# Performance work log

Measured on AMD Instinct MI355X. Metric: run time of the kernel, lower is better.

Reference implementation:

```python
import jax, jax.numpy as jnp
import numpy as np


def setup_inputs() -> dict:
    key = jax.random.key(0)
    ks = jax.random.split(key, 12)
    B, C, H, W = 8, 256, 64, 64
    inter = C // 8
    s = 0.05  # weight scale keeps q.k logits in a stable softmax range
    f32 = jnp.float32
    x = jax.random.normal(ks[0], (B, C, H, W), f32)
    Wq = jax.random.normal(ks[1], (inter, C), f32) * s
    bq = jnp.zeros((inter,), f32)
    Wk = jax.random.normal(ks[2], (inter, C), f32) * s
    bk = jnp.zeros((inter,), f32)
    Wv = jax.random.normal(ks[3], (C, C), f32) * s
    bv = jnp.zeros((C,), f32)
    gamma = jnp.full((1,), 0.5, f32)  # learnable residual scale (init 0 in torch; 0.5 exercises the path)
    Wg1 = jax.random.normal(ks[4], (inter, C), f32) * s
    bg1 = jnp.zeros((inter,), f32)
    Wg2 = jax.random.normal(ks[5], (C, inter), f32) * s
    bg2 = jnp.zeros((C,), f32)
    return {"x": x, "Wq": Wq, "bq": bq, "Wk": Wk, "bk": bk, "Wv": Wv, "bv": bv,
            "gamma": gamma, "Wg1": Wg1, "bg1": bg1, "Wg2": Wg2, "bg2": bg2}


def reference(x, Wq, bq, Wk, bk, Wv, bv, gamma, Wg1, bg1, Wg2, bg2):
    B, C, H, W = x.shape
    N = H * W
    xf = x.reshape(B, C, N)  # [B,C,N]
    # 1x1 convs == per-pixel linear projections
    q = jnp.einsum('oc,bcn->bon', Wq, xf) + bq[None, :, None]  # [B,inter,N]
    k = jnp.einsum('oc,bcn->bon', Wk, xf) + bk[None, :, None]  # [B,inter,N]
    v = jnp.einsum('oc,bcn->bon', Wv, xf) + bv[None, :, None]  # [B,C,N]
    # attention[b,n,m] = softmax_m( q[b,:,n] . k[b,:,m] )
    attn = jax.nn.softmax(jnp.einsum('bin,bim->bnm', q, k), axis=-1)  # [B,N,N]
    # out[b,c,n] = sum_m v[b,c,m] * attn[b,n,m]
    out = jnp.einsum('bcm,bnm->bcn', v, attn)  # [B,C,N]
    out = gamma[0] * out + xf
    # gated global pooling branch: GAP -> 1x1 conv -> ReLU -> 1x1 conv -> Sigmoid
    gp = xf.mean(axis=-1)  # [B,C]
    h = jax.nn.relu(jnp.einsum('oc,bc->bo', Wg1, gp) + bg1)  # [B,inter]
    ga = jax.nn.sigmoid(jnp.einsum('co,bo->bc', Wg2, h) + bg2)  # [B,C]
    out = out * ga[:, :, None] + out
    return out.reshape(B, C, H, W)
```

## Files before the change

kernel.cpp:

```cpp
#include <hip/hip_runtime.h>

typedef unsigned short u16;
typedef unsigned int   u32;
typedef short s16x4 __attribute__((ext_vector_type(4)));
typedef u16 u16x4 __attribute__((ext_vector_type(4)));
typedef u16 u16x8 __attribute__((ext_vector_type(8)));
typedef __bf16 bf16x8 __attribute__((ext_vector_type(8)));
typedef float f32x4 __attribute__((ext_vector_type(4)));
typedef float f32x2 __attribute__((ext_vector_type(2)));
typedef u32 u32x2v __attribute__((ext_vector_type(2)));
typedef u32 u32x4v __attribute__((ext_vector_type(4)));

#define NB 8
#define NC 256
#define NI 32
#define NN 4096
#define LOG2E 1.4426950408889634f
#define POFF 64.0f

#define OW_Q   0
#define OB_Q   8192
#define OW_K   8224
#define OB_K   16416
#define OW_V   16448
#define OB_V   81984
#define OGAM   82240
#define OW_G1  82248
#define OB_G1  90440
#define OW_G2  90472
#define OB_G2  98664
#define WTOT   98920

__device__ __forceinline__ float bf2f(u16 v) {
    u32 u = ((u32)v) << 16;
    return __builtin_bit_cast(float, u);
}
__device__ __forceinline__ u16 f2bf(float f) {
    u32 u = __builtin_bit_cast(u32, f);
    u32 lsb = (u >> 16) & 1u;
    u += 0x7fffu + lsb;
    return (u16)(u >> 16);
}
__device__ __forceinline__ u32 cvtpk_bf16(float lo, float hi) {
    u32 r;
    asm("v_cvt_pk_bf16_f32 %0, %1, %2" : "=v"(r) : "v"(lo), "v"(hi));
    return r;
}
__device__ __forceinline__ u16 f2bf_hw(float f) {
    u32 r;
    asm("v_cvt_pk_bf16_f32 %0, %1, %1" : "=v"(r) : "v"(f));
    return (u16)r;
}
__device__ __forceinline__ void permswap32(u32& a, u32& b) {
#if __has_builtin(__builtin_amdgcn_permlane32_swap)
    auto r = __builtin_amdgcn_permlane32_swap(a, b, false, false);
    a = (u32)r[0]; b = (u32)r[1];
#else
    int ln = (int)(threadIdx.x & 63);
    u32 a2 = (u32)__shfl_xor((int)a, 32, 64);
    u32 b2 = (u32)__shfl_xor((int)b, 32, 64);
    u32 na = (ln < 32) ? a : b2;
    u32 nb = (ln < 32) ? a2 : b;
    a = na; b = nb;
#endif
}
__device__ __forceinline__ void permswap16(u32& a, u32& b) {
#if __has_builtin(__builtin_amdgcn_permlane16_swap)
    auto r = __builtin_amdgcn_permlane16_swap(a, b, false, false);
    a = (u32)r[0]; b = (u32)r[1];
#else
    int q = (int)((threadIdx.x >> 4) & 1);
    u32 az = (u32)__shfl_xor((int)a, 16, 64);
    u32 bz = (u32)__shfl_xor((int)b, 16, 64);
    u32 na = q ? bz : a;
    u32 nb = q ? b  : az;
    a = na; b = nb;
#endif
}
__device__ __forceinline__ bool is_f32_mode(const void* graw) {
    return ((const u16*)graw)[0] == 0;
}

__global__ __launch_bounds__(256) void convert_kernel(
    const void* x,  const void* Wq, const void* bq, const void* Wk, const void* bk,
    const void* Wv, const void* bv, const void* gamma, const void* Wg1, const void* bg1,
    const void* Wg2, const void* bg2, float* __restrict__ xf, float* __restrict__ wbuf,
    u16* __restrict__ wbf, float* __restrict__ gp)
{
    bool f32m = is_f32_mode(gamma);
    int blk = blockIdx.x, t = threadIdx.x;
    if (blk < 2048) {
        int base = blk * 4096 + t * 16;
        float s = 0.f;
        if (f32m) {
            const float* xs = (const float*)x;
#pragma unroll
            for (int k = 0; k < 4; ++k) {
                f32x4 a = *(const f32x4*)(xs + base + k * 4);
                s += (a[0] + a[1]) + (a[2] + a[3]);
            }
        } else {
            const u16* xs = (const u16*)x;
#pragma unroll
            for (int k = 0; k < 2; ++k) {
                u16x8 a = *(const u16x8*)(xs + base + k * 8);
#pragma unroll
                for (int j = 0; j < 8; ++j) s += bf2f(a[j]);
            }
        }
#pragma unroll
        for (int off = 1; off <= 32; off <<= 1) s += __shfl_xor(s, off, 64);
        __shared__ float ws[4];
        if ((t & 63) == 0) ws[t >> 6] = s;
        __syncthreads();
        if (t == 0) gp[blk] = (ws[0] + ws[1] + ws[2] + ws[3]) * (1.0f / NN);
        return;
    }
    if (blk < 2080) {
        int tid = (blk - 2048) * 256 + t;
        const int off[12] = {OW_Q, OB_Q, OW_K, OB_K, OW_V, OB_V, OGAM, OW_G1, OB_G1, OW_G2, OB_G2, WTOT};
        const int len[11] = {8192, 32, 8192, 32, 65536, 256, 1, 8192, 32, 8192, 256};
        const void* srcs[11] = {Wq, bq, Wk, bk, Wv, bv, gamma, Wg1, bg1, Wg2, bg2};
        for (int w = tid; w < WTOT; w += 32 * 256) {
            int seg = 0;
#pragma unroll
            for (int i = 1; i < 11; ++i) if (w >= off[i]) seg = i;
            int idx = w - off[seg];
            float val = 0.f;
            if (idx < len[seg])
                val = f32m ? ((const float*)srcs[seg])[idx] : bf2f(((const u16*)srcs[seg])[idx]);
            wbuf[w] = val;
        }
        return;
    }
    int tid = (blk - 2080) * 256 + t;
    for (int w = tid; w < 320 * 256; w += 10 * 256) {
        int row = w >> 8, c = w & 255;
        const void* src; int idx; float scale = 1.f;
        if (row < 32)      { src = Wq; idx = row * 256 + c; scale = LOG2E; }
        else if (row < 64) { src = Wk; idx = (row - 32) * 256 + c; }
        else               { src = Wv; idx = (row - 64) * 256 + c; }
        float val = f32m ? ((const float*)src)[idx] : bf2f(((const u16*)src)[idx]);
        wbf[w] = f2bf(val * scale);
    }
}

__global__ __launch_bounds__(256) void proj_kernel(
    const void* xr, const float* __restrict__ xf, const void* graw,
    const float* __restrict__ wbuf, const u16* __restrict__ wbf,
    u16* __restrict__ qt, u16* __restrict__ kt, u16* __restrict__ v)
{
    __shared__ __attribute__((aligned(16))) u16 xs[64][264];

    bool f32m = is_f32_mode(graw);

    int t    = threadIdx.x;
    int lane = t & 63;
    int wave = t >> 6;
    int b    = blockIdx.x >> 6;
    int m0   = (blockIdx.x & 63) << 6;
    int l15  = lane & 15;
    int quad = lane >> 4;

    {
        int c0 = wave * 64;
        if (f32m) {
            const float* xb = (const float*)xr + (size_t)b * NC * NN + m0 + lane;
#pragma unroll
            for (int ci = 0; ci < 64; ci += 4) {
                int c = c0 + ci;
                float a0 = xb[(size_t)(c    ) * NN];
                float a1 = xb[(size_t)(c + 1) * NN];
                float a2 = xb[(size_t)(c + 2) * NN];
                float a3 = xb[(size_t)(c + 3) * NN];
                u32x2v p2;
                p2.x = cvtpk_bf16(a0, a1);
                p2.y = cvtpk_bf16(a2, a3);
                *(u32x2v*)&xs[lane][c] = p2;
            }
        } else {
            const u16* xb = (const u16*)xr + (size_t)b * NC * NN + m0 + lane;
#pragma unroll
            for (int ci = 0; ci < 64; ci += 4) {
                int c = c0 + ci;
                u16x4 p4;
                p4[0] = xb[(size_t)(c    ) * NN];
                p4[1] = xb[(size_t)(c + 1) * NN];
                p4[2] = xb[(size_t)(c + 2) * NN];
                p4[3] = xb[(size_t)(c + 3) * NN];
                *(u16x4*)&xs[lane][c] = p4;
            }
        }
    }
    __syncthreads();

    const f32x4 zero4 = {};
    f32x4 acc[5][4];
#pragma unroll
    for (int i = 0; i < 5; ++i)
#pragma unroll
        for (int mt = 0; mt < 4; ++mt) acc[i][mt] = zero4;

    int obase = wave * 80;
    const u16* wb = wbf + (size_t)(obase + l15) * 256 + quad * 8;

    bf16x8 af[5];
#pragma unroll
    for (int i = 0; i < 5; ++i)
        af[i] = *(const bf16x8*)(wb + (size_t)(i * 16) * 256);

#pragma unroll
    for (int kc = 0; kc < 8; ++kc) {
        bf16x8 afn[5], bfr[4];
        if (kc < 7) {
#pragma unroll
            for (int i = 0; i < 5; ++i)
                afn[i] = *(const bf16x8*)(wb + (size_t)(i * 16) * 256 + (kc + 1) * 32);
        }
#pragma unroll
        for (int mt = 0; mt < 4; ++mt)
            bfr[mt] = *(const bf16x8*)&xs[mt * 16 + l15][kc * 32 + quad * 8];
#pragma unroll
        for (int i = 0; i < 5; ++i)
#pragma unroll
            for (int mt = 0; mt < 4; ++mt)
                acc[i][mt] = __builtin_amdgcn_mfma_f32_16x16x32_bf16(af[i], bfr[mt], acc[i][mt], 0, 0, 0);
        if (kc < 7) {
#pragma unroll
            for (int i = 0; i < 5; ++i) af[i] = afn[i];
        }
    }

    __syncthreads();

    if (wave == 0) {
#pragma unroll
        for (int i = 0; i < 4; ++i) {
#pragma unroll
            for (int mt = 0; mt < 4; ++mt) {
                float tv[4];
#pragma unroll
                for (int r = 0; r < 4; ++r) {
                    int o = i * 16 + quad * 4 + r;
                    float bias = (o < 32) ? LOG2E * wbuf[OB_Q + o] : wbuf[OB_K + o - 32];
                    tv[r] = acc[i][mt][r] + bias;
                }
                u32x2v p2;
                p2.x = cvtpk_bf16(tv[0], tv[1]);
                p2.y = cvtpk_bf16(tv[2], tv[3]);
                *(u32x2v*)&xs[mt * 16 + l15][i * 16 + quad * 4] = p2;
            }
        }
        int m = m0 + lane;
        u16* qrow = qt + (size_t)(b * NN + m) * NI;
        u16* krow = kt + (size_t)(b * NN + m) * NI;
#pragma unroll
        for (int j = 0; j < 4; ++j) *(u16x8*)(qrow + j * 8) = *(const u16x8*)&xs[lane][j * 8];
#pragma unroll
        for (int j = 0; j < 4; ++j) *(u16x8*)(krow + j * 8) = *(const u16x8*)&xs[lane][32 + j * 8];
#pragma unroll
        for (int mt = 0; mt < 4; ++mt) {
#pragma unroll
            for (int r = 0; r < 4; ++r) {
                int c = quad * 4 + r;
                v[(size_t)(b * NC + c) * NN + m0 + mt * 16 + l15] = f2bf_hw(acc[4][mt][r] + wbuf[OB_V + c]);
            }
        }
    } else {
#pragma unroll
        for (int i = 0; i < 5; ++i) {
#pragma unroll
            for (int mt = 0; mt < 4; ++mt) {
#pragma unroll
                for (int r = 0; r < 4; ++r) {
                    int c = wave * 80 + i * 16 + quad * 4 + r - 64;
                    v[(size_t)(b * NC + c) * NN + m0 + mt * 16 + l15] = f2bf_hw(acc[i][mt][r] + wbuf[OB_V + c]);
                }
            }
        }
    }
}

__global__ __launch_bounds__(256) void gate_kernel(
    const float* __restrict__ gp, const float* __restrict__ wbuf, float* __restrict__ gmul)
{
    int b = blockIdx.x;
    int t = threadIdx.x;
    __shared__ float gps[NC];
    __shared__ float hs[NI];
    gps[t] = gp[b * NC + t];
    __syncthreads();
    if (t < NI) {
        float a = wbuf[OB_G1 + t];
        for (int c = 0; c < NC; ++c) a += wbuf[OW_G1 + t * NC + c] * gps[c];
        hs[t] = a > 0.f ? a : 0.f;
    }
    __syncthreads();
    float a = wbuf[OB_G2 + t];
#pragma unroll
    for (int i = 0; i < NI; ++i) a += wbuf[OW_G2 + t * NI + i] * hs[i];
    float sig = 1.f / (1.f + __expf(-a));
    gmul[b * NC + t] = 1.f + sig;
}

__global__ __launch_bounds__(512, 4) void flash_kernel(
    const u16* __restrict__ qt, const u16* __restrict__ kt, const u16* __restrict__ v,
    const void* xr, const float* __restrict__ xf, const void* graw,
    const float* __restrict__ wbuf, const float* __restrict__ gmul, void* outp)
{
    __shared__ __attribute__((aligned(16))) u16 vs[2][2][NC][40];

    bool f32m = is_f32_mode(graw);

    int t    = threadIdx.x;
    int lane = t & 63;
    int wave = t >> 6;
    int b    = blockIdx.x & 7;
    int nblk = (blockIdx.x >> 3) << 6;
    int n0   = nblk + (wave >> 1) * 16;
    int c0   = (wave & 1) * 128;
    int l15  = lane & 15;
    int quad = lane >> 4;

    const f32x4 mneg = {-POFF, -POFF, -POFF, -POFF};

    bf16x8 qf = *(const bf16x8*)(qt + (size_t)(b * NN + n0 + l15) * NI + quad * 8);

    f32x4 acc[8];
#pragma unroll
    for (int ct = 0; ct < 8; ++ct) acc[ct] = f32x4{};
    f32x2 psum2 = {};

    int sc = t >> 2;
    int sm = (t & 3) * 8;
    const u16* vb0 = v + (size_t)(b * NC + sc) * NN + sm;
    const u16* vb1 = v + (size_t)(b * NC + sc + 128) * NN + sm;
    const u16* ktb = kt + (size_t)(b * NN + l15) * NI + quad * 8;

    u16x8 sr0, sr1, sr2, sr3;
    sr0 = *(const u16x8*)(vb0);        sr1 = *(const u16x8*)(vb1);
    sr2 = *(const u16x8*)(vb0 + 32);   sr3 = *(const u16x8*)(vb1 + 32);
    *(u16x8*)&vs[0][0][sc][sm]       = sr0;
    *(u16x8*)&vs[0][0][sc + 128][sm] = sr1;
    *(u16x8*)&vs[0][1][sc][sm]       = sr2;
    *(u16x8*)&vs[0][1][sc + 128][sm] = sr3;
    sr0 = *(const u16x8*)(vb0 + 64);   sr1 = *(const u16x8*)(vb1 + 64);
    sr2 = *(const u16x8*)(vb0 + 96);   sr3 = *(const u16x8*)(vb1 + 96);
    bf16x8 ktA[2], ktB[2];
    ktA[0] = *(const bf16x8*)(ktb);
    ktA[1] = *(const bf16x8*)(ktb + (size_t)16 * NI);
    ktB[0] = *(const bf16x8*)(ktb + (size_t)32 * NI);
    ktB[1] = *(const bf16x8*)(ktb + (size_t)48 * NI);
    __syncthreads();

    for (int it = 0; it < 64; ++it) {
        int p = it & 1;
        bool wmore = (it < 63);
        bool lmore = (it < 62);

        if (wmore) {
            *(u16x8*)&vs[p ^ 1][0][sc][sm]       = sr0;
            *(u16x8*)&vs[p ^ 1][0][sc + 128][sm] = sr1;
            *(u16x8*)&vs[p ^ 1][1][sc][sm]       = sr2;
            *(u16x8*)&vs[p ^ 1][1][sc + 128][sm] = sr3;
        }
        if (lmore) {
            int cb = it * 64 + 128;
            sr0 = *(const u16x8*)(vb0 + cb);
            sr1 = *(const u16x8*)(vb1 + cb);
            sr2 = *(const u16x8*)(vb0 + cb + 32);
            sr3 = *(const u16x8*)(vb1 + cb + 32);
        }

#pragma unroll
        for (int h = 0; h < 2; ++h) {
            bf16x8* ktX = (h == 0) ? ktA : ktB;

            f32x4 sf[2];
#pragma unroll
            for (int mt = 0; mt < 2; ++mt)
                sf[mt] = __builtin_amdgcn_mfma_f32_16x16x32_bf16(ktX[mt], qf, mneg, 0, 0, 0);

            bf16x8 va8[8];
#pragma unroll
            for (int ct = 0; ct < 8; ++ct)
                va8[ct] = *(const bf16x8*)&vs[p][h][c0 + ct * 16 + l15][quad * 8];

            if (wmore) {
                int mg = it * 64 + 64 + h * 32;
                ktX[0] = *(const bf16x8*)(ktb + (size_t)mg * NI);
                ktX[1] = *(const bf16x8*)(ktb + (size_t)(mg + 16) * NI);
            }

            float pp[2][4];
#pragma unroll
            for (int mt = 0; mt < 2; ++mt)
#pragma unroll
                for (int r = 0; r < 4; ++r)
                    pp[mt][r] = __builtin_amdgcn_exp2f(sf[mt][r]);
            f32x2 t0; t0.x = pp[0][0]; t0.y = pp[0][1];
            f32x2 t1; t1.x = pp[0][2]; t1.y = pp[0][3];
            f32x2 t2; t2.x = pp[1][0]; t2.y = pp[1][1];
            f32x2 t3; t3.x = pp[1][2]; t3.y = pp[1][3];
            psum2 += (t0 + t1) + (t2 + t3);
            u32 A0 = cvtpk_bf16(pp[0][0], pp[0][1]);
            u32 A1 = cvtpk_bf16(pp[0][2], pp[0][3]);
            u32 B0 = cvtpk_bf16(pp[1][0], pp[1][1]);
            u32 B1 = cvtpk_bf16(pp[1][2], pp[1][3]);
            permswap32(A0, B0); permswap16(A0, B0);
            permswap32(A1, B1); permswap16(A1, B1);
            u32x4v f; f.x = A0; f.y = A1; f.z = B0; f.w = B1;
            bf16x8 pfr8 = __builtin_bit_cast(bf16x8, f);

#pragma unroll
            for (int ct = 0; ct < 8; ++ct)
                acc[ct] = __builtin_amdgcn_mfma_f32_16x16x32_bf16(va8[ct], pfr8, acc[ct], 0, 0, 0);
        }

        __syncthreads();
    }

    float s = psum2.x + psum2.y;
    s += __shfl_xor(s, 16, 64);
    s += __shfl_xor(s, 32, 64);
    float inv = 1.f / s;
    float gam = wbuf[OGAM];
    int n = n0 + l15;

#pragma unroll
    for (int ct = 0; ct < 8; ++ct) {
        int cb = c0 + ct * 16 + quad * 4;
        f32x4 gm4 = *(const f32x4*)&gmul[b * NC + cb];
#pragma unroll
        for (int r = 0; r < 4; ++r) {
            size_t off = (size_t)(b * NC + cb + r) * NN + n;
            float xv = f32m ? ((const float*)xr)[off] : bf2f(((const u16*)xr)[off]);
            float val = (gam * acc[ct][r] * inv + xv) * gm4[r];
            if (f32m) ((float*)outp)[off] = val;
            else      ((u16*)outp)[off]  = f2bf_hw(val);
        }
    }
}

extern "C" void kernel_launch(void* const* d_in, const int* in_sizes, int n_in,
                              void* d_out, int out_size, void* d_ws, size_t ws_size,
                              hipStream_t stream)
{
    const void* x     = d_in[0];
    const void* Wq    = d_in[1];
    const void* bq    = d_in[2];
    const void* Wk    = d_in[3];
    const void* bk    = d_in[4];
    const void* Wv    = d_in[5];
    const void* bvp   = d_in[6];
    const void* gamma = d_in[7];
    const void* Wg1   = d_in[8];
    const void* bg1   = d_in[9];
    const void* Wg2   = d_in[10];
    const void* bg2   = d_in[11];

    char* ws = (char*)d_ws;
    float* xf   = (float*)ws;
    float* wbuf = (float*)(ws + 33554432);
    u16*   qt   = (u16*)  (ws + 33951744);
    u16*   kt   = (u16*)  (ws + 36048896);
    u16*   v    = (u16*)  (ws + 38146048);
    float* gp   = (float*)(ws + 54923264);
    float* gmul = (float*)(ws + 54931456);
    u16*   wbf  = (u16*)  (ws + 54939648);

    convert_kernel<<<2090, 256, 0, stream>>>(x, Wq, bq, Wk, bk, Wv, bvp, gamma,
                                             Wg1, bg1, Wg2, bg2, xf, wbuf, wbf, gp);
    proj_kernel<<<NB * 64, 256, 0, stream>>>(x, xf, gamma, wbuf, wbf, qt, kt, v);
    gate_kernel<<<NB, 256, 0, stream>>>(gp, wbuf, gmul);
    flash_kernel<<<NB * 64, 512, 0, stream>>>(qt, kt, v, x, xf, gamma, wbuf, gmul, d_out);
}
```

Baseline: 257.9 us.

## Fold weight conversion and pooling into projection kernel, drop convert kernel

```diff
diff --git a/kernel.cpp b/kernel.cpp
--- a/kernel.cpp
+++ b/kernel.cpp
@@ -18,28 +18,9 @@
 #define LOG2E 1.4426950408889634f
 #define POFF 64.0f
 
-#define OW_Q   0
-#define OB_Q   8192
-#define OW_K   8224
-#define OB_K   16416
-#define OW_V   16448
-#define OB_V   81984
-#define OGAM   82240
-#define OW_G1  82248
-#define OB_G1  90440
-#define OW_G2  90472
-#define OB_G2  98664
-#define WTOT   98920
-
 __device__ __forceinline__ float bf2f(u16 v) {
     u32 u = ((u32)v) << 16;
     return __builtin_bit_cast(float, u);
-}
-__device__ __forceinline__ u16 f2bf(float f) {
-    u32 u = __builtin_bit_cast(u32, f);
-    u32 lsb = (u >> 16) & 1u;
-    u += 0x7fffu + lsb;
-    return (u16)(u >> 16);
 }
 __device__ __forceinline__ u32 cvtpk_bf16(float lo, float hi) {
     u32 r;
@@ -80,27 +61,41 @@
 __device__ __forceinline__ bool is_f32_mode(const void* graw) {
     return ((const u16*)graw)[0] == 0;
 }
-
-__global__ __launch_bounds__(256) void convert_kernel(
-    const void* x,  const void* Wq, const void* bq, const void* Wk, const void* bk,
-    const void* Wv, const void* bv, const void* gamma, const void* Wg1, const void* bg1,
-    const void* Wg2, const void* bg2, float* __restrict__ xf, float* __restrict__ wbuf,
-    u16* __restrict__ wbf, float* __restrict__ gp)
+__device__ __forceinline__ float ldb(bool f32m, const void* p, int idx) {
+    return f32m ? ((const float*)p)[idx] : bf2f(((const u16*)p)[idx]);
+}
+__device__ __forceinline__ bf16x8 ldwf(const float* p) {
+    f32x4 a = *(const f32x4*)p;
+    f32x4 c = *(const f32x4*)(p + 4);
+    u32x4v r;
+    r.x = cvtpk_bf16(a[0], a[1]); r.y = cvtpk_bf16(a[2], a[3]);
+    r.z = cvtpk_bf16(c[0], c[1]); r.w = cvtpk_bf16(c[2], c[3]);
+    return __builtin_bit_cast(bf16x8, r);
+}
+
+__global__ __launch_bounds__(256) void proj_kernel(
+    const void* xr, const void* graw,
+    const void* Wq, const void* bq, const void* Wk, const void* bk,
+    const void* Wv, const void* bv,
+    u16* __restrict__ qt, u16* __restrict__ kt, u16* __restrict__ v,
+    float* __restrict__ gp)
 {
-    bool f32m = is_f32_mode(gamma);
-    int blk = blockIdx.x, t = threadIdx.x;
-    if (blk < 2048) {
-        int base = blk * 4096 + t * 16;
+    bool f32m = is_f32_mode(graw);
+    int t = threadIdx.x;
+
+    if (blockIdx.x >= 512) {
+        int row = blockIdx.x - 512;
+        int base = row * 4096 + t * 16;
         float s = 0.f;
         if (f32m) {
-            const float* xs = (const float*)x;
+            const float* xs = (const float*)xr;
 #pragma unroll
             for (int k = 0; k < 4; ++k) {
                 f32x4 a = *(const f32x4*)(xs + base + k * 4);
                 s += (a[0] + a[1]) + (a[2] + a[3]);
             }
         } else {
-            const u16* xs = (const u16*)x;
+            const u16* xs = (const u16*)xr;
 #pragma unroll
             for (int k = 0; k < 2; ++k) {
                 u16x8 a = *(const u16x8*)(xs + base + k * 8);
@@ -113,48 +108,12 @@
         __shared__ float ws[4];
         if ((t & 63) == 0) ws[t >> 6] = s;
         __syncthreads();
-        if (t == 0) gp[blk] = (ws[0] + ws[1] + ws[2] + ws[3]) * (1.0f / NN);
+        if (t == 0) gp[row] = (ws[0] + ws[1] + ws[2] + ws[3]) * (1.0f / NN);
         return;
     }
-    if (blk < 2080) {
-        int tid = (blk - 2048) * 256 + t;
-        const int off[12] = {OW_Q, OB_Q, OW_K, OB_K, OW_V, OB_V, OGAM, OW_G1, OB_G1, OW_G2, OB_G2, WTOT};
-        const int len[11] = {8192, 32, 8192, 32, 65536, 256, 1, 8192, 32, 8192, 256};
-        const void* srcs[11] = {Wq, bq, Wk, bk, Wv, bv, gamma, Wg1, bg1, Wg2, bg2};
-        for (int w = tid; w < WTOT; w += 32 * 256) {
-            int seg = 0;
-#pragma unroll
-            for (int i = 1; i < 11; ++i) if (w >= off[i]) seg = i;
-            int idx = w - off[seg];
-            float val = 0.f;
-            if (idx < len[seg])
-                val = f32m ? ((const float*)srcs[seg])[idx] : bf2f(((const u16*)srcs[seg])[idx]);
-            wbuf[w] = val;
-        }
-        return;
-    }
-    int tid = (blk - 2080) * 256 + t;
-    for (int w = tid; w < 320 * 256; w += 10 * 256) {
-        int row = w >> 8, c = w & 255;
-        const void* src; int idx; float scale = 1.f;
-        if (row < 32)      { src = Wq; idx = row * 256 + c; scale = LOG2E; }
-        else if (row < 64) { src = Wk; idx = (row - 32) * 256 + c; }
-        else               { src = Wv; idx = (row - 64) * 256 + c; }
-        float val = f32m ? ((const float*)src)[idx] : bf2f(((const u16*)src)[idx]);
-        wbf[w] = f2bf(val * scale);
-    }
-}
-
-__global__ __launch_bounds__(256) void proj_kernel(
-    const void* xr, const float* __restrict__ xf, const void* graw,
-    const float* __restrict__ wbuf, const u16* __restrict__ wbf,
-    u16* __restrict__ qt, u16* __restrict__ kt, u16* __restrict__ v)
-{
+
     __shared__ __attribute__((aligned(16))) u16 xs[64][264];
 
-    bool f32m = is_f32_mode(graw);
-
-    int t    = threadIdx.x;
     int lane = t & 63;
     int wave = t >> 6;
     int b    = blockIdx.x >> 6;
@@ -202,12 +161,31 @@
         for (int mt = 0; mt < 4; ++mt) acc[i][mt] = zero4;
 
     int obase = wave * 80;
-    const u16* wb = wbf + (size_t)(obase + l15) * 256 + quad * 8;
+
+    const u16*   wsrc16[5];
+    const float* wsrc32[5];
+#pragma unroll
+    for (int i = 0; i < 5; ++i) {
+        int R0 = obase + i * 16;
+        if (f32m) {
+            const float* s = (R0 < 32) ? (const float*)Wq + (size_t)R0 * 256
+                           : (R0 < 64) ? (const float*)Wk + (size_t)(R0 - 32) * 256
+                                       : (const float*)Wv + (size_t)(R0 - 64) * 256;
+            wsrc32[i] = s + l15 * 256 + quad * 8;
+            wsrc16[i] = nullptr;
+        } else {
+            const u16* s = (R0 < 32) ? (const u16*)Wq + (size_t)R0 * 256
+                         : (R0 < 64) ? (const u16*)Wk + (size_t)(R0 - 32) * 256
+                                     : (const u16*)Wv + (size_t)(R0 - 64) * 256;
+            wsrc16[i] = s + l15 * 256 + quad * 8;
+            wsrc32[i] = nullptr;
+        }
+    }
 
     bf16x8 af[5];
 #pragma unroll
     for (int i = 0; i < 5; ++i)
-        af[i] = *(const bf16x8*)(wb + (size_t)(i * 16) * 256);
+        af[i] = f32m ? ldwf(wsrc32[i]) : *(const bf16x8*)(wsrc16[i]);
 
 #pragma unroll
     for (int kc = 0; kc < 8; ++kc) {
@@ -215,7 +193,8 @@
         if (kc < 7) {
 #pragma unroll
             for (int i = 0; i < 5; ++i)
-                afn[i] = *(const bf16x8*)(wb + (size_t)(i * 16) * 256 + (kc + 1) * 32);
+                afn[i] = f32m ? ldwf(wsrc32[i] + (kc + 1) * 32)
+                              : *(const bf16x8*)(wsrc16[i] + (kc + 1) * 32);
         }
 #pragma unroll
         for (int mt = 0; mt < 4; ++mt)
@@ -242,8 +221,8 @@
 #pragma unroll
                 for (int r = 0; r < 4; ++r) {
                     int o = i * 16 + quad * 4 + r;
-                    float bias = (o < 32) ? LOG2E * wbuf[OB_Q + o] : wbuf[OB_K + o - 32];
-                    tv[r] = acc[i][mt][r] + bias;
+                    if (o < 32) tv[r] = LOG2E * (acc[i][mt][r] + ldb(f32m, bq, o));
+                    else        tv[r] = acc[i][mt][r] + ldb(f32m, bk, o - 32);
                 }
                 u32x2v p2;
                 p2.x = cvtpk_bf16(tv[0], tv[1]);
@@ -263,7 +242,7 @@
 #pragma unroll
             for (int r = 0; r < 4; ++r) {
                 int c = quad * 4 + r;
-                v[(size_t)(b * NC + c) * NN + m0 + mt * 16 + l15] = f2bf_hw(acc[4][mt][r] + wbuf[OB_V + c]);
+                v[(size_t)(b * NC + c) * NN + m0 + mt * 16 + l15] = f2bf_hw(acc[4][mt][r] + ldb(f32m, bv, c));
             }
         }
     } else {
@@ -274,7 +253,7 @@
 #pragma unroll
                 for (int r = 0; r < 4; ++r) {
                     int c = wave * 80 + i * 16 + quad * 4 + r - 64;
-                    v[(size_t)(b * NC + c) * NN + m0 + mt * 16 + l15] = f2bf_hw(acc[i][mt][r] + wbuf[OB_V + c]);
+                    v[(size_t)(b * NC + c) * NN + m0 + mt * 16 + l15] = f2bf_hw(acc[i][mt][r] + ldb(f32m, bv, c));
                 }
             }
         }
@@ -282,8 +261,11 @@
 }
 
 __global__ __launch_bounds__(256) void gate_kernel(
-    const float* __restrict__ gp, const float* __restrict__ wbuf, float* __restrict__ gmul)
+    const float* __restrict__ gp, const void* graw,
+    const void* Wg1, const void* bg1, const void* Wg2, const void* bg2,
+    float* __restrict__ gmul)
 {
+    bool f32m = is_f32_mode(graw);
     int b = blockIdx.x;
     int t = threadIdx.x;
     __shared__ float gps[NC];
@@ -291,22 +273,22 @@
     gps[t] = gp[b * NC + t];
     __syncthreads();
     if (t < NI) {
-        float a = wbuf[OB_G1 + t];
-        for (int c = 0; c < NC; ++c) a += wbuf[OW_G1 + t * NC + c] * gps[c];
+        float a = ldb(f32m, bg1, t);
+        for (int c = 0; c < NC; ++c) a += ldb(f32m, Wg1, t * NC + c) * gps[c];
         hs[t] = a > 0.f ? a : 0.f;
     }
     __syncthreads();
-    float a = wbuf[OB_G2 + t];
-#pragma unroll
-    for (int i = 0; i < NI; ++i) a += wbuf[OW_G2 + t * NI + i] * hs[i];
+    float a = ldb(f32m, bg2, t);
+#pragma unroll
+    for (int i = 0; i < NI; ++i) a += ldb(f32m, Wg2, t * NI + i) * hs[i];
     float sig = 1.f / (1.f + __expf(-a));
     gmul[b * NC + t] = 1.f + sig;
 }
 
 __global__ __launch_bounds__(512, 4) void flash_kernel(
     const u16* __restrict__ qt, const u16* __restrict__ kt, const u16* __restrict__ v,
-    const void* xr, const float* __restrict__ xf, const void* graw,
-    const float* __restrict__ wbuf, const float* __restrict__ gmul, void* outp)
+    const void* xr, const void* graw,
+    const float* __restrict__ gmul, void* outp)
 {
     __shared__ __attribute__((aligned(16))) u16 vs[2][2][NC][40];
 
@@ -424,7 +406,7 @@
     s += __shfl_xor(s, 16, 64);
     s += __shfl_xor(s, 32, 64);
     float inv = 1.f / s;
-    float gam = wbuf[OGAM];
+    float gam = f32m ? ((const float*)graw)[0] : bf2f(((const u16*)graw)[0]);
     int n = n0 + l15;
 
 #pragma unroll
@@ -460,18 +442,14 @@
     const void* bg2   = d_in[11];
 
     char* ws = (char*)d_ws;
-    float* xf   = (float*)ws;
-    float* wbuf = (float*)(ws + 33554432);
     u16*   qt   = (u16*)  (ws + 33951744);
     u16*   kt   = (u16*)  (ws + 36048896);
     u16*   v    = (u16*)  (ws + 38146048);
     float* gp   = (float*)(ws + 54923264);
     float* gmul = (float*)(ws + 54931456);
-    u16*   wbf  = (u16*)  (ws + 54939648);
-
-    convert_kernel<<<2090, 256, 0, stream>>>(x, Wq, bq, Wk, bk, Wv, bvp, gamma,
-                                             Wg1, bg1, Wg2, bg2, xf, wbuf, wbf, gp);
-    proj_kernel<<<NB * 64, 256, 0, stream>>>(x, xf, gamma, wbuf, wbf, qt, kt, v);
-    gate_kernel<<<NB, 256, 0, stream>>>(gp, wbuf, gmul);
-    flash_kernel<<<NB * 64, 512, 0, stream>>>(qt, kt, v, x, xf, gamma, wbuf, gmul, d_out);
-}
+
+    proj_kernel<<<2560, 256, 0, stream>>>(x, gamma, Wq, bq, Wk, bk, Wv, bvp,
+                                          qt, kt, v, gp);
+    gate_kernel<<<NB, 256, 0, stream>>>(gp, gamma, Wg1, bg1, Wg2, bg2, gmul);
+    flash_kernel<<<NB * 64, 512, 0, stream>>>(qt, kt, v, x, gamma, gmul, d_out);
+}
```

After: 277.4 us. 1.08x slower.

## Load part of V tile directly from global into registers, bypass LDS

Applied to the files above, without the earlier changes.

```diff
diff --git a/kernel.cpp b/kernel.cpp
--- a/kernel.cpp
+++ b/kernel.cpp
@@ -308,7 +308,7 @@
     const void* xr, const float* __restrict__ xf, const void* graw,
     const float* __restrict__ wbuf, const float* __restrict__ gmul, void* outp)
 {
-    __shared__ __attribute__((aligned(16))) u16 vs[2][2][NC][40];
+    __shared__ __attribute__((aligned(16))) u16 vs[2][2][160][40];
 
     bool f32m = is_f32_mode(graw);
 
@@ -319,6 +319,7 @@
     int nblk = (blockIdx.x >> 3) << 6;
     int n0   = nblk + (wave >> 1) * 16;
     int c0   = (wave & 1) * 128;
+    int rb   = (wave & 1) * 80;
     int l15  = lane & 15;
     int quad = lane >> 4;
 
@@ -331,26 +332,39 @@
     for (int ct = 0; ct < 8; ++ct) acc[ct] = f32x4{};
     f32x2 psum2 = {};
 
-    int sc = t >> 2;
     int sm = (t & 3) * 8;
-    const u16* vb0 = v + (size_t)(b * NC + sc) * NN + sm;
-    const u16* vb1 = v + (size_t)(b * NC + sc + 128) * NN + sm;
+    int r1 = t >> 2;
+    int c1 = r1 + (r1 < 80 ? 0 : 48);
+    bool st2 = (wave < 2);
+    int r2 = 128 + (t >> 2);
+    int c2 = st2 ? (r2 + 48) : c1;
+    const u16* vp1 = v + (size_t)(b * NC + c1) * NN + sm;
+    const u16* vp2 = v + (size_t)(b * NC + c2) * NN + sm;
     const u16* ktb = kt + (size_t)(b * NN + l15) * NI + quad * 8;
-
-    u16x8 sr0, sr1, sr2, sr3;
-    sr0 = *(const u16x8*)(vb0);        sr1 = *(const u16x8*)(vb1);
-    sr2 = *(const u16x8*)(vb0 + 32);   sr3 = *(const u16x8*)(vb1 + 32);
-    *(u16x8*)&vs[0][0][sc][sm]       = sr0;
-    *(u16x8*)&vs[0][0][sc + 128][sm] = sr1;
-    *(u16x8*)&vs[0][1][sc][sm]       = sr2;
-    *(u16x8*)&vs[0][1][sc + 128][sm] = sr3;
-    sr0 = *(const u16x8*)(vb0 + 64);   sr1 = *(const u16x8*)(vb1 + 64);
-    sr2 = *(const u16x8*)(vb0 + 96);   sr3 = *(const u16x8*)(vb1 + 96);
+    const u16* vg0 = v + (size_t)(b * NC + c0 +  80 + l15) * NN + quad * 8;
+    const u16* vg1 = v + (size_t)(b * NC + c0 +  96 + l15) * NN + quad * 8;
+    const u16* vg2 = v + (size_t)(b * NC + c0 + 112 + l15) * NN + quad * 8;
+
+    u16x8 s10, s11, s20 = {}, s21 = {};
+    s10 = *(const u16x8*)(vp1);        s11 = *(const u16x8*)(vp1 + 32);
+    if (st2) { s20 = *(const u16x8*)(vp2);  s21 = *(const u16x8*)(vp2 + 32); }
+    *(u16x8*)&vs[0][0][r1][sm] = s10;
+    *(u16x8*)&vs[0][1][r1][sm] = s11;
+    if (st2) {
+        *(u16x8*)&vs[0][0][r2][sm] = s20;
+        *(u16x8*)&vs[0][1][r2][sm] = s21;
+    }
+    s10 = *(const u16x8*)(vp1 + 64);   s11 = *(const u16x8*)(vp1 + 96);
+    if (st2) { s20 = *(const u16x8*)(vp2 + 64); s21 = *(const u16x8*)(vp2 + 96); }
     bf16x8 ktA[2], ktB[2];
     ktA[0] = *(const bf16x8*)(ktb);
     ktA[1] = *(const bf16x8*)(ktb + (size_t)16 * NI);
     ktB[0] = *(const bf16x8*)(ktb + (size_t)32 * NI);
     ktB[1] = *(const bf16x8*)(ktb + (size_t)48 * NI);
+    bf16x8 vgA[3], vgB[3];
+    vgA[0] = *(const bf16x8*)(vg0);      vgB[0] = *(const bf16x8*)(vg0 + 32);
+    vgA[1] = *(const bf16x8*)(vg1);      vgB[1] = *(const bf16x8*)(vg1 + 32);
+    vgA[2] = *(const bf16x8*)(vg2);      vgB[2] = *(const bf16x8*)(vg2 + 32);
     __syncthreads();
 
     for (int it = 0; it < 64; ++it) {
@@ -359,32 +373,37 @@
         bool lmore = (it < 62);
 
         if (wmore) {
-            *(u16x8*)&vs[p ^ 1][0][sc][sm]       = sr0;
-            *(u16x8*)&vs[p ^ 1][0][sc + 128][sm] = sr1;
-            *(u16x8*)&vs[p ^ 1][1][sc][sm]       = sr2;
-            *(u16x8*)&vs[p ^ 1][1][sc + 128][sm] = sr3;
+            *(u16x8*)&vs[p ^ 1][0][r1][sm] = s10;
+            *(u16x8*)&vs[p ^ 1][1][r1][sm] = s11;
+            if (st2) {
+                *(u16x8*)&vs[p ^ 1][0][r2][sm] = s20;
+                *(u16x8*)&vs[p ^ 1][1][r2][sm] = s21;
+            }
         }
         if (lmore) {
             int cb = it * 64 + 128;
-            sr0 = *(const u16x8*)(vb0 + cb);
-            sr1 = *(const u16x8*)(vb1 + cb);
-            sr2 = *(const u16x8*)(vb0 + cb + 32);
-            sr3 = *(const u16x8*)(vb1 + cb + 32);
+            s10 = *(const u16x8*)(vp1 + cb);
+            s11 = *(const u16x8*)(vp1 + cb + 32);
+            if (st2) {
+                s20 = *(const u16x8*)(vp2 + cb);
+                s21 = *(const u16x8*)(vp2 + cb + 32);
+            }
         }
 
 #pragma unroll
         for (int h = 0; h < 2; ++h) {
             bf16x8* ktX = (h == 0) ? ktA : ktB;
+            bf16x8* vgX = (h == 0) ? vgA : vgB;
 
             f32x4 sf[2];
 #pragma unroll
             for (int mt = 0; mt < 2; ++mt)
                 sf[mt] = __builtin_amdgcn_mfma_f32_16x16x32_bf16(ktX[mt], qf, mneg, 0, 0, 0);
 
-            bf16x8 va8[8];
-#pragma unroll
-            for (int ct = 0; ct < 8; ++ct)
-                va8[ct] = *(const bf16x8*)&vs[p][h][c0 + ct * 16 + l15][quad * 8];
+            bf16x8 va8[5];
+#pragma unroll
+            for (int ct = 0; ct < 5; ++ct)
+                va8[ct] = *(const bf16x8*)&vs[p][h][rb + ct * 16 + l15][quad * 8];
 
             if (wmore) {
                 int mg = it * 64 + 64 + h * 32;
@@ -413,8 +432,18 @@
             bf16x8 pfr8 = __builtin_bit_cast(bf16x8, f);
 
 #pragma unroll
-            for (int ct = 0; ct < 8; ++ct)
+            for (int ct = 0; ct < 5; ++ct)
                 acc[ct] = __builtin_amdgcn_mfma_f32_16x16x32_bf16(va8[ct], pfr8, acc[ct], 0, 0, 0);
+#pragma unroll
+            for (int j = 0; j < 3; ++j)
+                acc[5 + j] = __builtin_amdgcn_mfma_f32_16x16x32_bf16(vgX[j], pfr8, acc[5 + j], 0, 0, 0);
+
+            if (wmore) {
+                int mg = it * 64 + 64 + h * 32;
+                vgX[0] = *(const bf16x8*)(vg0 + mg);
+                vgX[1] = *(const bf16x8*)(vg1 + mg);
+                vgX[2] = *(const bf16x8*)(vg2 + mg);
+            }
         }
 
         __syncthreads();
```

Result: slower. 437.5 us (+69.6%).
